# Kernel tuning notes

Hardware: AMD Instinct MI355X
Metric: run time of the kernel (lower is better)

The kernel has to match this reference:

```python
import jax, jax.numpy as jnp
import numpy as np
from jax import lax

B, LATENT, SEQ, HID, OUT = 4096, 128, 512, 32, 64


def setup_inputs() -> dict:
    key = jax.random.key(0)
    ks = jax.random.split(key, 9)
    s = 1.0 / np.sqrt(HID)  # PyTorch-style init scale
    f32 = jnp.float32
    return {
        "z": jax.random.normal(ks[0], (B, LATENT), f32),
        "init_W": jax.random.uniform(ks[1], (HID, LATENT), f32, -s, s),
        "init_b": jax.random.uniform(ks[2], (HID,), f32, -s, s),
        "W_ih": jax.random.uniform(ks[3], (4 * HID, HID), f32, -s, s),
        "W_hh": jax.random.uniform(ks[4], (4 * HID, HID), f32, -s, s),
        "b_ih": jax.random.uniform(ks[5], (4 * HID,), f32, -s, s),
        "b_hh": jax.random.uniform(ks[6], (4 * HID,), f32, -s, s),
        "out_W": jax.random.uniform(ks[7], (OUT, HID), f32, -s, s),
        "out_b": jax.random.uniform(ks[8], (OUT,), f32, -s, s),
    }


def reference(z, init_W, init_b, W_ih, W_hh, b_ih, b_hh, out_W, out_b):
    # init_fc: z -> h0 (num_layers=1); cell starts at zero
    h0 = z @ init_W.T + init_b  # [B, H]
    c0 = jnp.zeros_like(h0)

    # x_in is all zeros, so the input-to-hidden term is a constant bias;
    # compute it once (keeps W_ih in the graph, matmul with zeros == 0).
    x_zero = jnp.zeros((z.shape[0], W_ih.shape[1]), z.dtype)
    gate_const = x_zero @ W_ih.T + b_ih + b_hh  # [B, 4H]

    def step(carry, _):
        h, c = carry
        gates = h @ W_hh.T + gate_const  # [B, 4H], PyTorch gate order i,f,g,o
        i, f, g, o = jnp.split(gates, 4, axis=-1)
        i = jax.nn.sigmoid(i)
        f = jax.nn.sigmoid(f)
        g = jnp.tanh(g)
        o = jax.nn.sigmoid(o)
        c = f * c + i * g
        h = o * jnp.tanh(c)
        return (h, c), h

    _, hs = lax.scan(step, (h0, c0), None, length=SEQ)  # [T, B, H]
    out = jnp.transpose(hs, (1, 0, 2))  # [B, T, H] (batch_first)
    y = out @ out_W.T + out_b  # [B, T, OUT]
    return y
```

## Files before the change

### kernel.cpp

```cpp
#include <hip/hip_runtime.h>


#define B_SZ   4096
#define LATENT 128
#define SEQ    512
#define HID    32
#define OUT_N  64
#define ROWS   16
#define LSW    40

typedef _Float16 f16x8 __attribute__((ext_vector_type(8)));
typedef _Float16 f16x4 __attribute__((ext_vector_type(4)));
typedef float    f32x4 __attribute__((ext_vector_type(4)));

__device__ __forceinline__ float fexp2(float x) { return __builtin_amdgcn_exp2f(x); }
__device__ __forceinline__ float frcp(float x)  { return __builtin_amdgcn_rcpf(x); }
__device__ __forceinline__ float tanh_f(float x) {
    return fmaf(-2.f, frcp(1.f + fexp2(2.88539008177792681f * x)), 1.f);
}
__device__ __forceinline__ void lds_barrier() {
    asm volatile("s_waitcnt lgkmcnt(0)\n\ts_barrier" ::: "memory");
}

__global__ __launch_bounds__(512)
void lstm_tr10(const float* __restrict__ z,
               const float* __restrict__ init_W,
               const float* __restrict__ init_b,
               const float* __restrict__ W_hh,
               const float* __restrict__ b_ih,
               const float* __restrict__ b_hh,
               const float* __restrict__ out_W,
               const float* __restrict__ out_b,
               float* __restrict__ y)
{
    __shared__ __align__(16) _Float16 hst[ROWS * LSW];
    __shared__ __align__(16) unsigned short hx2[2][64][8];

    const int tid  = threadIdx.x;
    const int w    = tid >> 6;
    const int lane = tid & 63;
    const int n_   = lane & 15;
    const int kb   = lane >> 4;
    const int jj   = w & 1;
    const int r_   = w >> 1;
    const int rbase = blockIdx.x * ROWS;

    const float NL2E = -1.44269504088896341f;
    const float P2L2E = 2.88539008177792681f;

    f16x8 wf1;
    f32x4 bacc1;
    {
        const int arow = 32 * (n_ & 3) + 16 * jj + 4 * (n_ >> 2) + r_;
        const float asc = ((n_ & 3) == 2) ? P2L2E : NL2E;
        const float* wrow = W_hh + (size_t)arow * HID;
#pragma unroll
        for (int rr = 0; rr < 4; rr++) {
            wf1[rr]     = (_Float16)(asc * wrow[4 * kb + rr]);
            wf1[4 + rr] = (_Float16)(asc * wrow[16 + 4 * kb + rr]);
        }
#pragma unroll
        for (int r = 0; r < 4; r++) {
            const int G = 32 * r + 16 * jj + 4 * kb + r_;
            const float bsc = (r == 2) ? P2L2E : NL2E;
            bacc1[r] = bsc * (b_ih[G] + b_hh[G]);
        }
    }

    f16x8 owf;
    f32x4 oacc;
    {
        const int p = r_;
        const float* row = out_W + (size_t)(16 * p + n_) * HID;
#pragma unroll
        for (int rr = 0; rr < 4; rr++) {
            owf[rr]     = (_Float16)row[4 * kb + rr];
            owf[4 + rr] = (_Float16)row[4 * kb + 16 + rr];
        }
#pragma unroll
        for (int r = 0; r < 4; r++) oacc[r] = out_b[16 * p + 4 * kb + r];
    }

    {
        int m = tid >> 5, j = tid & 31;
        const float4* zp = (const float4*)(z + (size_t)(rbase + m) * LATENT);
        const float4* wp = (const float4*)(init_W + (size_t)j * LATENT);
        float acc = init_b[j];
#pragma unroll
        for (int k = 0; k < LATENT / 4; k++) {
            float4 a4 = zp[k], b4 = wp[k];
            acc = fmaf(a4.x, b4.x, acc); acc = fmaf(a4.y, b4.y, acc);
            acc = fmaf(a4.z, b4.z, acc); acc = fmaf(a4.w, b4.w, acc);
        }
        hst[m * LSW + j] = (_Float16)acc;
    }
    __syncthreads();

    f16x8 a;
    {
        f16x4 lo = *(const f16x4*)&hst[n_ * LSW + 4 * kb];
        f16x4 hi = *(const f16x4*)&hst[n_ * LSW + 4 * kb + 16];
#pragma unroll
        for (int r = 0; r < 4; r++) { a[r] = lo[r]; a[4 + r] = hi[r]; }
    }

    float c1 = 0.f;

    float* yb = y + (size_t)(rbase + n_) * SEQ * OUT_N + 16 * r_ + 4 * kb;

    for (int t = 0; t < SEQ; t += 4) {
#pragma unroll
        for (int u = 0; u < 4; u++) {
            const int par = u & 1;
            f32x4 acc = __builtin_amdgcn_mfma_f32_16x16x32_f16(wf1, a, bacc1, 0, 0, 0);

            {
                float gi = frcp(1.f + fexp2(acc[0]));
                float gf = frcp(1.f + fexp2(acc[1]));
                float gg = fmaf(-2.f, frcp(1.f + fexp2(acc[2])), 1.f);
                float go = frcp(1.f + fexp2(acc[3]));
                float cn = fmaf(gf, c1, gi * gg);
                c1 = cn;
                union { _Float16 h; unsigned short u16; } cv;
                cv.h = (_Float16)(go * tanh_f(cn));
                hx2[par][lane][4 * jj + r_] = cv.u16;
            }
            lds_barrier();

            a = *(const f16x8*)&hx2[par][lane][0];

            if (jj == par) {
                f32x4 py = __builtin_amdgcn_mfma_f32_16x16x32_f16(owf, a, oacc, 0, 0, 0);
                *(f32x4*)(yb + (size_t)(t + u) * OUT_N) = py;
            }
        }
    }
}

extern "C" void kernel_launch(void* const* d_in, const int* in_sizes, int n_in,
                              void* d_out, int out_size, void* d_ws, size_t ws_size,
                              hipStream_t stream) {
    const float* z      = (const float*)d_in[0];
    const float* init_W = (const float*)d_in[1];
    const float* init_b = (const float*)d_in[2];
    const float* W_hh   = (const float*)d_in[4];
    const float* b_ih   = (const float*)d_in[5];
    const float* b_hh   = (const float*)d_in[6];
    const float* out_W  = (const float*)d_in[7];
    const float* out_b  = (const float*)d_in[8];
    float* yout = (float*)d_out;

    lstm_tr10<<<B_SZ / ROWS, 512, 0, stream>>>(z, init_W, init_b, W_hh, b_ih, b_hh,
                                               out_W, out_b, yout);
}
```

Before: 605.0 us.

## Defer output projection off the recurrence path, pad LDS h exchange, fold tanh scaling

The output-projection MFMA for step s-1 is now issued right after the gate MFMA of step s, instead of after the barrier. This takes it off the serial recurrence critical path and lets it overlap with the gate math. The final timestep is projected after the loop. The LDS exchange rows are padded from 8 to 10 halves, presumably to reduce bank conflicts. Because the padded rows are no longer 16-byte aligned, each row is read as four dword loads. The cell state is kept pre-scaled by 2·log2(e), which removes one multiply from the tanh(c) path at the cost of slightly different rounding.

```diff
diff --git a/kernel.cpp b/kernel.cpp
--- a/kernel.cpp
+++ b/kernel.cpp
@@ -8,6 +8,7 @@
 #define OUT_N  64
 #define ROWS   16
 #define LSW    40
+#define HXW    10
 
 typedef _Float16 f16x8 __attribute__((ext_vector_type(8)));
 typedef _Float16 f16x4 __attribute__((ext_vector_type(4)));
@@ -15,15 +16,12 @@
 
 __device__ __forceinline__ float fexp2(float x) { return __builtin_amdgcn_exp2f(x); }
 __device__ __forceinline__ float frcp(float x)  { return __builtin_amdgcn_rcpf(x); }
-__device__ __forceinline__ float tanh_f(float x) {
-    return fmaf(-2.f, frcp(1.f + fexp2(2.88539008177792681f * x)), 1.f);
-}
 __device__ __forceinline__ void lds_barrier() {
     asm volatile("s_waitcnt lgkmcnt(0)\n\ts_barrier" ::: "memory");
 }
 
 __global__ __launch_bounds__(512)
-void lstm_tr10(const float* __restrict__ z,
+void lstm_tr11(const float* __restrict__ z,
                const float* __restrict__ init_W,
                const float* __restrict__ init_b,
                const float* __restrict__ W_hh,
@@ -34,7 +32,7 @@
                float* __restrict__ y)
 {
     __shared__ __align__(16) _Float16 hst[ROWS * LSW];
-    __shared__ __align__(16) unsigned short hx2[2][64][8];
+    __shared__ __align__(16) unsigned short hx2[2][64][HXW];
 
     const int tid  = threadIdx.x;
     const int w    = tid >> 6;
@@ -45,8 +43,8 @@
     const int r_   = w >> 1;
     const int rbase = blockIdx.x * ROWS;
 
-    const float NL2E = -1.44269504088896341f;
-    const float P2L2E = 2.88539008177792681f;
+    const float NL2E  = -1.44269504088896341f;
+    const float P2L2E =  2.88539008177792681f;
 
     f16x8 wf1;
     f32x4 bacc1;
@@ -104,7 +102,7 @@
         for (int r = 0; r < 4; r++) { a[r] = lo[r]; a[4 + r] = hi[r]; }
     }
 
-    float c1 = 0.f;
+    float cs = 0.f;
 
     float* yb = y + (size_t)(rbase + n_) * SEQ * OUT_N + 16 * r_ + 4 * kb;
 
@@ -114,26 +112,39 @@
             const int par = u & 1;
             f32x4 acc = __builtin_amdgcn_mfma_f32_16x16x32_f16(wf1, a, bacc1, 0, 0, 0);
 
+            if (jj == par) {
+                f32x4 py = __builtin_amdgcn_mfma_f32_16x16x32_f16(owf, a, oacc, 0, 0, 0);
+                if (t + u) *(f32x4*)(yb + (size_t)(t + u - 1) * OUT_N) = py;
+            }
+
             {
                 float gi = frcp(1.f + fexp2(acc[0]));
                 float gf = frcp(1.f + fexp2(acc[1]));
-                float gg = fmaf(-2.f, frcp(1.f + fexp2(acc[2])), 1.f);
+                float rg = frcp(1.f + fexp2(acc[2]));
                 float go = frcp(1.f + fexp2(acc[3]));
-                float cn = fmaf(gf, c1, gi * gg);
-                c1 = cn;
+                float g2 = fmaf(-2.f * P2L2E, rg, P2L2E);
+                float csn = fmaf(gf, cs, gi * g2);
+                cs = csn;
+                float rt = frcp(1.f + fexp2(csn));
+                float hh = fmaf(-2.f * go, rt, go);
                 union { _Float16 h; unsigned short u16; } cv;
-                cv.h = (_Float16)(go * tanh_f(cn));
+                cv.h = (_Float16)hh;
                 hx2[par][lane][4 * jj + r_] = cv.u16;
             }
             lds_barrier();
 
-            a = *(const f16x8*)&hx2[par][lane][0];
-
-            if (jj == par) {
-                f32x4 py = __builtin_amdgcn_mfma_f32_16x16x32_f16(owf, a, oacc, 0, 0, 0);
-                *(f32x4*)(yb + (size_t)(t + u) * OUT_N) = py;
+            {
+                union { unsigned int u[4]; f16x8 v; } ua;
+                const unsigned int* rp = (const unsigned int*)&hx2[par][lane][0];
+                ua.u[0] = rp[0]; ua.u[1] = rp[1]; ua.u[2] = rp[2]; ua.u[3] = rp[3];
+                a = ua.v;
             }
         }
+    }
+
+    if (jj == 0) {
+        f32x4 py = __builtin_amdgcn_mfma_f32_16x16x32_f16(owf, a, oacc, 0, 0, 0);
+        *(f32x4*)(yb + (size_t)(SEQ - 1) * OUT_N) = py;
     }
 }
 
@@ -150,6 +161,6 @@
     const float* out_b  = (const float*)d_in[8];
     float* yout = (float*)d_out;
 
-    lstm_tr10<<<B_SZ / ROWS, 512, 0, stream>>>(z, init_W, init_b, W_hh, b_ih, b_hh,
+    lstm_tr11<<<B_SZ / ROWS, 512, 0, stream>>>(z, init_W, init_b, W_hh, b_ih, b_hh,
                                                out_W, out_b, yout);
 }
```

Result: faster. 583.5 us (-3.6%).

## Run each 16-row LSTM tile in a single wavefront, dropping LDS barriers

Applied to the files above, without the earlier changes.

The old kernel split each 16-row batch tile across 8 waves, each computing one gate slice, and exchanged hidden state through LDS with a barrier every timestep. The new kernel gives the whole tile to one 64-lane wave. That wave holds all 8 gate weight fragments and 4 output fragments in registers and issues 8 recurrent MFMAs plus 4 output MFMAs per step, so the MFMA accumulator layout feeds the next step's operand directly with no LDS traffic or barrier. The tanh scaling is folded into the fused gate arithmetic. The cost is more serial work per wave (8 MFMAs plus 8 cell updates per step on the critical path) and far fewer threads per block, which lowers parallelism and latency hiding.

```diff
diff --git a/kernel.cpp b/kernel.cpp
--- a/kernel.cpp
+++ b/kernel.cpp
@@ -7,23 +7,15 @@
 #define HID    32
 #define OUT_N  64
 #define ROWS   16
-#define LSW    40
 
 typedef _Float16 f16x8 __attribute__((ext_vector_type(8)));
-typedef _Float16 f16x4 __attribute__((ext_vector_type(4)));
 typedef float    f32x4 __attribute__((ext_vector_type(4)));
 
 __device__ __forceinline__ float fexp2(float x) { return __builtin_amdgcn_exp2f(x); }
 __device__ __forceinline__ float frcp(float x)  { return __builtin_amdgcn_rcpf(x); }
-__device__ __forceinline__ float tanh_f(float x) {
-    return fmaf(-2.f, frcp(1.f + fexp2(2.88539008177792681f * x)), 1.f);
-}
-__device__ __forceinline__ void lds_barrier() {
-    asm volatile("s_waitcnt lgkmcnt(0)\n\ts_barrier" ::: "memory");
-}
 
-__global__ __launch_bounds__(512)
-void lstm_tr10(const float* __restrict__ z,
+__global__ __launch_bounds__(64)
+void lstm_wl12(const float* __restrict__ z,
                const float* __restrict__ init_W,
                const float* __restrict__ init_b,
                const float* __restrict__ W_hh,
@@ -33,106 +25,108 @@
                const float* __restrict__ out_b,
                float* __restrict__ y)
 {
-    __shared__ __align__(16) _Float16 hst[ROWS * LSW];
-    __shared__ __align__(16) unsigned short hx2[2][64][8];
-
-    const int tid  = threadIdx.x;
-    const int w    = tid >> 6;
-    const int lane = tid & 63;
+    const int lane = threadIdx.x;
     const int n_   = lane & 15;
-    const int kb   = lane >> 4;
-    const int jj   = w & 1;
-    const int r_   = w >> 1;
+    const int q    = lane >> 4;
     const int rbase = blockIdx.x * ROWS;
 
-    const float NL2E = -1.44269504088896341f;
-    const float P2L2E = 2.88539008177792681f;
+    const float NL2E  = -1.44269504088896341f;
+    const float P2L2E =  2.88539008177792681f;
 
-    f16x8 wf1;
-    f32x4 bacc1;
-    {
-        const int arow = 32 * (n_ & 3) + 16 * jj + 4 * (n_ >> 2) + r_;
-        const float asc = ((n_ & 3) == 2) ? P2L2E : NL2E;
-        const float* wrow = W_hh + (size_t)arow * HID;
+    f16x8 wf[8];
+    f32x4 bacc[8];
 #pragma unroll
-        for (int rr = 0; rr < 4; rr++) {
-            wf1[rr]     = (_Float16)(asc * wrow[4 * kb + rr]);
-            wf1[4 + rr] = (_Float16)(asc * wrow[16 + 4 * kb + rr]);
-        }
+    for (int s = 0; s < 2; s++) {
 #pragma unroll
-        for (int r = 0; r < 4; r++) {
-            const int G = 32 * r + 16 * jj + 4 * kb + r_;
-            const float bsc = (r == 2) ? P2L2E : NL2E;
-            bacc1[r] = bsc * (b_ih[G] + b_hh[G]);
+        for (int G = 0; G < 4; G++) {
+            const int t = 4 * s + G;
+            const float sc = (G == 2) ? P2L2E : NL2E;
+            const float* row = W_hh + (size_t)(32 * G + 16 * s + n_) * HID;
+            f16x8 v;
+#pragma unroll
+            for (int rr = 0; rr < 4; rr++) {
+                v[rr]     = (_Float16)(sc * row[4 * q + rr]);
+                v[4 + rr] = (_Float16)(sc * row[16 + 4 * q + rr]);
+            }
+            wf[t] = v;
+            f32x4 b;
+#pragma unroll
+            for (int r = 0; r < 4; r++) {
+                const int gr = 32 * G + 16 * s + 4 * q + r;
+                b[r] = sc * (b_ih[gr] + b_hh[gr]);
+            }
+            bacc[t] = b;
         }
     }
 
-    f16x8 owf;
-    f32x4 oacc;
-    {
-        const int p = r_;
+    f16x8 owf[4];
+    f32x4 oacc[4];
+#pragma unroll
+    for (int p = 0; p < 4; p++) {
         const float* row = out_W + (size_t)(16 * p + n_) * HID;
+        f16x8 v;
 #pragma unroll
         for (int rr = 0; rr < 4; rr++) {
-            owf[rr]     = (_Float16)row[4 * kb + rr];
-            owf[4 + rr] = (_Float16)row[4 * kb + 16 + rr];
+            v[rr]     = (_Float16)row[4 * q + rr];
+            v[4 + rr] = (_Float16)row[16 + 4 * q + rr];
         }
+        owf[p] = v;
 #pragma unroll
-        for (int r = 0; r < 4; r++) oacc[r] = out_b[16 * p + 4 * kb + r];
+        for (int r = 0; r < 4; r++) oacc[p][r] = out_b[16 * p + 4 * q + r];
     }
 
+    f16x8 a;
+    float cs[8];
     {
-        int m = tid >> 5, j = tid & 31;
-        const float4* zp = (const float4*)(z + (size_t)(rbase + m) * LATENT);
-        const float4* wp = (const float4*)(init_W + (size_t)j * LATENT);
-        float acc = init_b[j];
+        const float4* zp = (const float4*)(z + (size_t)(rbase + n_) * LATENT);
 #pragma unroll
-        for (int k = 0; k < LATENT / 4; k++) {
-            float4 a4 = zp[k], b4 = wp[k];
-            acc = fmaf(a4.x, b4.x, acc); acc = fmaf(a4.y, b4.y, acc);
-            acc = fmaf(a4.z, b4.z, acc); acc = fmaf(a4.w, b4.w, acc);
+        for (int s = 0; s < 2; s++) {
+#pragma unroll
+            for (int r = 0; r < 4; r++) {
+                const int c = 16 * s + 4 * q + r;
+                const float4* wp = (const float4*)(init_W + (size_t)c * LATENT);
+                float acc0 = init_b[c];
+#pragma unroll 8
+                for (int k = 0; k < LATENT / 4; k++) {
+                    float4 a4 = zp[k], b4 = wp[k];
+                    acc0 = fmaf(a4.x, b4.x, acc0); acc0 = fmaf(a4.y, b4.y, acc0);
+                    acc0 = fmaf(a4.z, b4.z, acc0); acc0 = fmaf(a4.w, b4.w, acc0);
+                }
+                a[4 * s + r] = (_Float16)acc0;
+                cs[4 * s + r] = 0.f;
+            }
         }
-        hst[m * LSW + j] = (_Float16)acc;
-    }
-    __syncthreads();
-
-    f16x8 a;
-    {
-        f16x4 lo = *(const f16x4*)&hst[n_ * LSW + 4 * kb];
-        f16x4 hi = *(const f16x4*)&hst[n_ * LSW + 4 * kb + 16];
-#pragma unroll
-        for (int r = 0; r < 4; r++) { a[r] = lo[r]; a[4 + r] = hi[r]; }
     }
 
-    float c1 = 0.f;
+    float* yb = y + (size_t)(rbase + n_) * SEQ * OUT_N + 4 * q;
 
-    float* yb = y + (size_t)(rbase + n_) * SEQ * OUT_N + 16 * r_ + 4 * kb;
+    for (int it = 0; it < SEQ; it++) {
+        f32x4 acc[8];
+#pragma unroll
+        for (int t = 0; t < 8; t++)
+            acc[t] = __builtin_amdgcn_mfma_f32_16x16x32_f16(wf[t], a, bacc[t], 0, 0, 0);
 
-    for (int t = 0; t < SEQ; t += 4) {
 #pragma unroll
-        for (int u = 0; u < 4; u++) {
-            const int par = u & 1;
-            f32x4 acc = __builtin_amdgcn_mfma_f32_16x16x32_f16(wf1, a, bacc1, 0, 0, 0);
+        for (int s = 0; s < 2; s++) {
+#pragma unroll
+            for (int r = 0; r < 4; r++) {
+                const int i8 = 4 * s + r;
+                float gi = frcp(1.f + fexp2(acc[4 * s + 0][r]));
+                float gf = frcp(1.f + fexp2(acc[4 * s + 1][r]));
+                float rg = frcp(1.f + fexp2(acc[4 * s + 2][r]));
+                float go = frcp(1.f + fexp2(acc[4 * s + 3][r]));
+                float g2 = fmaf(-2.f * P2L2E, rg, P2L2E);
+                float csn = fmaf(gf, cs[i8], gi * g2);
+                cs[i8] = csn;
+                float rt = frcp(1.f + fexp2(csn));
+                a[i8] = (_Float16)fmaf(-2.f * go, rt, go);
+            }
+        }
 
-            {
-                float gi = frcp(1.f + fexp2(acc[0]));
-                float gf = frcp(1.f + fexp2(acc[1]));
-                float gg = fmaf(-2.f, frcp(1.f + fexp2(acc[2])), 1.f);
-                float go = frcp(1.f + fexp2(acc[3]));
-                float cn = fmaf(gf, c1, gi * gg);
-                c1 = cn;
-                union { _Float16 h; unsigned short u16; } cv;
-                cv.h = (_Float16)(go * tanh_f(cn));
-                hx2[par][lane][4 * jj + r_] = cv.u16;
-            }
-            lds_barrier();
-
-            a = *(const f16x8*)&hx2[par][lane][0];
-
-            if (jj == par) {
-                f32x4 py = __builtin_amdgcn_mfma_f32_16x16x32_f16(owf, a, oacc, 0, 0, 0);
-                *(f32x4*)(yb + (size_t)(t + u) * OUT_N) = py;
-            }
+#pragma unroll
+        for (int p = 0; p < 4; p++) {
+            f32x4 py = __builtin_amdgcn_mfma_f32_16x16x32_f16(owf[p], a, oacc[p], 0, 0, 0);
+            *(f32x4*)(yb + (size_t)it * OUT_N + 16 * p) = py;
         }
     }
 }
@@ -150,6 +144,6 @@
     const float* out_b  = (const float*)d_in[8];
     float* yout = (float*)d_out;
 
-    lstm_tr10<<<B_SZ / ROWS, 512, 0, stream>>>(z, init_W, init_b, W_hh, b_ih, b_hh,
-                                               out_W, out_b, yout);
+    lstm_wl12<<<B_SZ / ROWS, 64, 0, stream>>>(z, init_W, init_b, W_hh, b_ih, b_hh,
+                                              out_W, out_b, yout);
 }
```

Measured after the change: 788.0 us. +30.3%, slower.

## Specialize warps into recurrence and output-projection roles

Applied to the files above, without the earlier changes.

The eight waves are split into four recurrence waves, each running two MFMAs and two LSTM cell updates per step, and four output waves that only run the output projection and store to global memory. Previously every wave did one cell update, and half of them also did the projection on alternating steps. The LDS exchange buffer is padded to a stride of 10 and written as packed 32-bit pairs, and the tanh math is folded into fewer FMAs. This aims to keep the output stores off the recurrence critical path, at the cost of doubling transcendental work per recurrence wave.

```diff
diff --git a/kernel.cpp b/kernel.cpp
--- a/kernel.cpp
+++ b/kernel.cpp
@@ -8,6 +8,7 @@
 #define OUT_N  64
 #define ROWS   16
 #define LSW    40
+#define HXW    10
 
 typedef _Float16 f16x8 __attribute__((ext_vector_type(8)));
 typedef _Float16 f16x4 __attribute__((ext_vector_type(4)));
@@ -15,15 +16,12 @@
 
 __device__ __forceinline__ float fexp2(float x) { return __builtin_amdgcn_exp2f(x); }
 __device__ __forceinline__ float frcp(float x)  { return __builtin_amdgcn_rcpf(x); }
-__device__ __forceinline__ float tanh_f(float x) {
-    return fmaf(-2.f, frcp(1.f + fexp2(2.88539008177792681f * x)), 1.f);
-}
 __device__ __forceinline__ void lds_barrier() {
     asm volatile("s_waitcnt lgkmcnt(0)\n\ts_barrier" ::: "memory");
 }
 
 __global__ __launch_bounds__(512)
-void lstm_tr10(const float* __restrict__ z,
+void lstm_ws13(const float* __restrict__ z,
                const float* __restrict__ init_W,
                const float* __restrict__ init_b,
                const float* __restrict__ W_hh,
@@ -34,51 +32,58 @@
                float* __restrict__ y)
 {
     __shared__ __align__(16) _Float16 hst[ROWS * LSW];
-    __shared__ __align__(16) unsigned short hx2[2][64][8];
+    __shared__ __align__(4) unsigned short hx[2][64][HXW];
 
     const int tid  = threadIdx.x;
     const int w    = tid >> 6;
     const int lane = tid & 63;
     const int n_   = lane & 15;
-    const int kb   = lane >> 4;
-    const int jj   = w & 1;
-    const int r_   = w >> 1;
+    const int q    = lane >> 4;
     const int rbase = blockIdx.x * ROWS;
+    const bool isrec = (w < 4);
 
-    const float NL2E = -1.44269504088896341f;
-    const float P2L2E = 2.88539008177792681f;
+    const float NL2E  = -1.44269504088896341f;
+    const float P2L2E =  2.88539008177792681f;
 
-    f16x8 wf1;
-    f32x4 bacc1;
-    {
-        const int arow = 32 * (n_ & 3) + 16 * jj + 4 * (n_ >> 2) + r_;
-        const float asc = ((n_ & 3) == 2) ? P2L2E : NL2E;
-        const float* wrow = W_hh + (size_t)arow * HID;
+    const int s_  = (w >> 1) & 1;
+    const int p0  = w & 1;
+    f16x8 wf0, wf1;
+    f32x4 bacc0, bacc1;
+    if (isrec) {
 #pragma unroll
-        for (int rr = 0; rr < 4; rr++) {
-            wf1[rr]     = (_Float16)(asc * wrow[4 * kb + rr]);
-            wf1[4 + rr] = (_Float16)(asc * wrow[16 + 4 * kb + rr]);
-        }
+        for (int m = 0; m < 2; m++) {
+            const int arow = 32 * (n_ & 3) + 16 * s_ + 4 * (n_ >> 2) + 2 * p0 + m;
+            const float asc = ((n_ & 3) == 2) ? P2L2E : NL2E;
+            const float* wrow = W_hh + (size_t)arow * HID;
+            f16x8 v;
 #pragma unroll
-        for (int r = 0; r < 4; r++) {
-            const int G = 32 * r + 16 * jj + 4 * kb + r_;
-            const float bsc = (r == 2) ? P2L2E : NL2E;
-            bacc1[r] = bsc * (b_ih[G] + b_hh[G]);
+            for (int rr = 0; rr < 4; rr++) {
+                v[rr]     = (_Float16)(asc * wrow[4 * q + rr]);
+                v[4 + rr] = (_Float16)(asc * wrow[16 + 4 * q + rr]);
+            }
+            f32x4 b;
+#pragma unroll
+            for (int r = 0; r < 4; r++) {
+                const int G = 32 * r + 16 * s_ + 4 * q + 2 * p0 + m;
+                const float bsc = (r == 2) ? P2L2E : NL2E;
+                b[r] = bsc * (b_ih[G] + b_hh[G]);
+            }
+            if (m == 0) { wf0 = v; bacc0 = b; } else { wf1 = v; bacc1 = b; }
         }
     }
 
     f16x8 owf;
     f32x4 oacc;
-    {
-        const int p = r_;
+    if (!isrec) {
+        const int p = w - 4;
         const float* row = out_W + (size_t)(16 * p + n_) * HID;
 #pragma unroll
         for (int rr = 0; rr < 4; rr++) {
-            owf[rr]     = (_Float16)row[4 * kb + rr];
-            owf[4 + rr] = (_Float16)row[4 * kb + 16 + rr];
+            owf[rr]     = (_Float16)row[4 * q + rr];
+            owf[4 + rr] = (_Float16)row[16 + 4 * q + rr];
         }
 #pragma unroll
-        for (int r = 0; r < 4; r++) oacc[r] = out_b[16 * p + 4 * kb + r];
+        for (int r = 0; r < 4; r++) oacc[r] = out_b[16 * p + 4 * q + r];
     }
 
     {
@@ -97,39 +102,62 @@
     __syncthreads();
 
     f16x8 a;
-    {
-        f16x4 lo = *(const f16x4*)&hst[n_ * LSW + 4 * kb];
-        f16x4 hi = *(const f16x4*)&hst[n_ * LSW + 4 * kb + 16];
+    if (isrec) {
+        f16x4 lo = *(const f16x4*)&hst[n_ * LSW + 4 * q];
+        f16x4 hi = *(const f16x4*)&hst[n_ * LSW + 4 * q + 16];
 #pragma unroll
         for (int r = 0; r < 4; r++) { a[r] = lo[r]; a[4 + r] = hi[r]; }
     }
 
-    float c1 = 0.f;
+    float cs0 = 0.f, cs1 = 0.f;
 
-    float* yb = y + (size_t)(rbase + n_) * SEQ * OUT_N + 16 * r_ + 4 * kb;
+    float* yb = y + (size_t)(rbase + n_) * SEQ * OUT_N + 16 * (w - 4) + 4 * q;
 
     for (int t = 0; t < SEQ; t += 4) {
 #pragma unroll
         for (int u = 0; u < 4; u++) {
             const int par = u & 1;
-            f32x4 acc = __builtin_amdgcn_mfma_f32_16x16x32_f16(wf1, a, bacc1, 0, 0, 0);
+            if (isrec) {
+                f32x4 ac0 = __builtin_amdgcn_mfma_f32_16x16x32_f16(wf0, a, bacc0, 0, 0, 0);
+                f32x4 ac1 = __builtin_amdgcn_mfma_f32_16x16x32_f16(wf1, a, bacc1, 0, 0, 0);
 
-            {
-                float gi = frcp(1.f + fexp2(acc[0]));
-                float gf = frcp(1.f + fexp2(acc[1]));
-                float gg = fmaf(-2.f, frcp(1.f + fexp2(acc[2])), 1.f);
-                float go = frcp(1.f + fexp2(acc[3]));
-                float cn = fmaf(gf, c1, gi * gg);
-                c1 = cn;
-                union { _Float16 h; unsigned short u16; } cv;
-                cv.h = (_Float16)(go * tanh_f(cn));
-                hx2[par][lane][4 * jj + r_] = cv.u16;
-            }
-            lds_barrier();
+                float gi0 = frcp(1.f + fexp2(ac0[0]));
+                float gf0 = frcp(1.f + fexp2(ac0[1]));
+                float rg0 = frcp(1.f + fexp2(ac0[2]));
+                float go0 = frcp(1.f + fexp2(ac0[3]));
+                float g20 = fmaf(-2.f * P2L2E, rg0, P2L2E);
+                float cn0 = fmaf(gf0, cs0, gi0 * g20);
+                cs0 = cn0;
+                float rt0 = frcp(1.f + fexp2(cn0));
+                float h0v = fmaf(-2.f * go0, rt0, go0);
+                float gi1 = frcp(1.f + fexp2(ac1[0]));
+                float gf1 = frcp(1.f + fexp2(ac1[1]));
+                float rg1 = frcp(1.f + fexp2(ac1[2]));
+                float go1 = frcp(1.f + fexp2(ac1[3]));
+                float g21 = fmaf(-2.f * P2L2E, rg1, P2L2E);
+                float cn1 = fmaf(gf1, cs1, gi1 * g21);
+                cs1 = cn1;
+                float rt1 = frcp(1.f + fexp2(cn1));
+                float h1v = fmaf(-2.f * go1, rt1, go1);
 
-            a = *(const f16x8*)&hx2[par][lane][0];
+                union { _Float16 h[2]; unsigned u32; } cv;
+                cv.h[0] = (_Float16)h0v;
+                cv.h[1] = (_Float16)h1v;
+                *(unsigned*)&hx[par][lane][4 * s_ + 2 * p0] = cv.u32;
 
-            if (jj == par) {
+                lds_barrier();
+
+                union { unsigned u[4]; f16x8 v; } ua;
+                const unsigned* rp = (const unsigned*)&hx[par][lane][0];
+                ua.u[0] = rp[0]; ua.u[1] = rp[1]; ua.u[2] = rp[2]; ua.u[3] = rp[3];
+                a = ua.v;
+            } else {
+                lds_barrier();
+
+                union { unsigned u[4]; f16x8 v; } ua;
+                const unsigned* rp = (const unsigned*)&hx[par][lane][0];
+                ua.u[0] = rp[0]; ua.u[1] = rp[1]; ua.u[2] = rp[2]; ua.u[3] = rp[3];
+                a = ua.v;
                 f32x4 py = __builtin_amdgcn_mfma_f32_16x16x32_f16(owf, a, oacc, 0, 0, 0);
                 *(f32x4*)(yb + (size_t)(t + u) * OUT_N) = py;
             }
@@ -150,6 +178,6 @@
     const float* out_b  = (const float*)d_in[8];
     float* yout = (float*)d_out;
 
-    lstm_tr10<<<B_SZ / ROWS, 512, 0, stream>>>(z, init_W, init_b, W_hh, b_ih, b_hh,
+    lstm_ws13<<<B_SZ / ROWS, 512, 0, stream>>>(z, init_W, init_b, W_hh, b_ih, b_hh,
                                                out_W, out_b, yout);
 }
```

New measurement: 603.1 us. Within noise of the previous version (-0.3%).
